# Optimization experiments

Hardware: AMD Instinct MI355X
Metric: run time of the kernel (lower is better)

## Reference

```python
import jax, jax.numpy as jnp
import numpy as np

DIM = 192
HEADS = 6
HIDDEN = 384  # int(DIM * 2.0)


def _ln(x, w, b):
    # WithBias LayerNorm over channel dim (torch normalizes last dim of b,(hw),c)
    mu = jnp.mean(x, axis=1, keepdims=True)
    var = jnp.var(x, axis=1, keepdims=True)
    return (x - mu) / jnp.sqrt(var + 1e-5) * w[None, :, None, None] + b[None, :, None, None]


def _conv1x1(x, w):  # w: [O, I, 1, 1]
    return jnp.einsum('bihw,oi->bohw', x, w[:, :, 0, 0])


def _dwconv3(x, w):  # depthwise 3x3, w: [C, 1, 3, 3]
    return jax.lax.conv_general_dilated(
        x, w, window_strides=(1, 1), padding=((1, 1), (1, 1)),
        feature_group_count=x.shape[1],
        dimension_numbers=('NCHW', 'OIHW', 'NCHW'))


def _l2norm(x):  # F.normalize along last axis
    n = jnp.sqrt(jnp.sum(x * x, axis=-1, keepdims=True))
    return x / jnp.maximum(n, 1e-12)


def setup_inputs() -> dict:
    key = jax.random.key(0)
    ks = jax.random.split(key, 16)
    s = 0.02
    d = {}
    d['x'] = jax.random.normal(ks[0], (2, DIM, 128, 128), dtype=jnp.float32)
    d['k_v'] = jax.random.normal(ks[1], (2, 256), dtype=jnp.float32)
    d['ln1_w'] = jnp.ones((DIM,), jnp.float32)
    d['ln1_b'] = jnp.zeros((DIM,), jnp.float32)
    d['temp'] = jnp.ones((HEADS, 1, 1), jnp.float32)
    d['w_kR'] = jax.random.normal(ks[2], (DIM * 3 // 4, 192), jnp.float32) * s
    d['w_kI'] = jax.random.normal(ks[3], (DIM // 4, 64), jnp.float32) * s
    d['w_qR'] = jax.random.normal(ks[4], (DIM, DIM * 3 // 4, 1, 1), jnp.float32) * s
    d['w_qdw'] = jax.random.normal(ks[5], (DIM, 1, 3, 3), jnp.float32) * s
    d['w_kvI'] = jax.random.normal(ks[6], (DIM * 2, DIM // 4, 1, 1), jnp.float32) * s
    d['w_kvdw'] = jax.random.normal(ks[7], (DIM * 2, 1, 3, 3), jnp.float32) * s
    d['w_po'] = jax.random.normal(ks[8], (DIM, DIM, 1, 1), jnp.float32) * s
    d['ln2_w'] = jnp.ones((DIM,), jnp.float32)
    d['ln2_b'] = jnp.zeros((DIM,), jnp.float32)
    d['w_ffk'] = jax.random.normal(ks[9], (DIM, 256), jnp.float32) * s
    d['w_pin'] = jax.random.normal(ks[10], (HIDDEN * 2, DIM, 1, 1), jnp.float32) * s
    d['w_dw'] = jax.random.normal(ks[11], (HIDDEN * 2, 1, 3, 3), jnp.float32) * s
    d['w_pout'] = jax.random.normal(ks[12], (DIM, HIDDEN, 1, 1), jnp.float32) * s
    return d


def reference(x, k_v, ln1_w, ln1_b, temp, w_kR, w_kI, w_qR, w_qdw, w_kvI, w_kvdw,
              w_po, ln2_w, ln2_b, w_ffk, w_pin, w_dw, w_pout):
    b, c, h, w = x.shape
    c3 = c * 3 // 4
    # ---- Rttention on norm1(x) ----
    xn = _ln(x, ln1_w, ln1_b)
    kvr = (k_v[:, :192] @ w_kR.T)[:, :, None, None]   # [b, 3c/4, 1, 1]
    kvi = (k_v[:, 192:] @ w_kI.T)[:, :, None, None]   # [b, c/4, 1, 1]
    x_r = xn[:, :c3] * kvr + xn[:, :c3]
    x_i = xn[:, c3:] * kvi + xn[:, c3:]
    q = _dwconv3(_conv1x1(x_r, w_qR), w_qdw)          # [b, c, h, w]
    kv = _dwconv3(_conv1x1(x_i, w_kvI), w_kvdw)       # [b, 2c, h, w]
    k, v = jnp.split(kv, 2, axis=1)
    rh = lambda t: t.reshape(b, HEADS, c // HEADS, h * w)
    q = _l2norm(rh(q))
    k = _l2norm(rh(k))
    v = rh(v)
    # channel-wise attention: [b, head, c_h, c_h]
    attn = jax.nn.softmax(jnp.einsum('bhcd,bhed->bhce', q, k) * temp[None], axis=-1)
    out = jnp.einsum('bhce,bhed->bhcd', attn, v).reshape(b, c, h, w)
    x = x + _conv1x1(out, w_po)
    # ---- GDFN FeedForward on norm2(x) ----
    xn2 = _ln(x, ln2_w, ln2_b)
    kvf = (k_v @ w_ffk.T)[:, :, None, None]           # [b, c, 1, 1]
    y = xn2 * kvf + xn2
    y = _dwconv3(_conv1x1(y, w_pin), w_dw)            # [b, 2*hidden, h, w]
    y1, y2 = jnp.split(y, 2, axis=1)
    y = jax.nn.gelu(y1, approximate=False) * y2
    x = x + _conv1x1(y, w_pout)
    return (x, k_v)
```

## Files before the change

kernel.cpp:

```cpp
#include <hip/hip_runtime.h>
#include <math.h>

#define HW 16384
#define CDIM 192
#define C3 144
#define C4 48
#define NB 2
#define NPX 32768
#define HEADS 6

typedef unsigned short u16;
typedef unsigned int u32;
typedef __attribute__((ext_vector_type(8))) short bf16x8;
typedef __attribute__((ext_vector_type(4))) float f32x4;

__device__ __forceinline__ float bf2f(u16 u) {
    return __uint_as_float(((unsigned int)u) << 16);
}
__device__ __forceinline__ u16 f2bf(float f) {
    unsigned int x = __float_as_uint(f);
    unsigned int r = x + 0x7fffu + ((x >> 16) & 1u);
    return (u16)(r >> 16);
}

static inline float* wsf(void* ws, size_t off) { return (float*)((char*)ws + off); }
static inline u16* wsh(void* ws, size_t off) { return (u16*)((char*)ws + off); }

__global__ void k_setup(const float* __restrict__ kvv, const float* __restrict__ wkR,
                        const float* __restrict__ wkI, const float* __restrict__ wffk,
                        const float* __restrict__ wqR, const float* __restrict__ wkvI,
                        const float* __restrict__ wpo, const float* __restrict__ wpin,
                        const float* __restrict__ wpout,
                        const float* __restrict__ ln2w, const float* __restrict__ ln2b,
                        u16* __restrict__ wb, float* __restrict__ sm,
                        float* __restrict__ A2, float* __restrict__ B2,
                        float* __restrict__ tail) {
    int t = blockIdx.x * 256 + threadIdx.x;
    if (t < 313344) {
        float v;
        if (t < 30720) {
            int o = t / 160, i = t % 160;
            v = (i < 144) ? wqR[o * 144 + i] : 0.f;
        } else if (t < 55296) {
            int r = t - 30720; int o = r / 64, i = r % 64;
            v = (i < 48) ? wkvI[o * 48 + i] : 0.f;
        } else if (t < 92160) {
            v = wpo[t - 55296];
        } else if (t < 239616) {
            v = wpin[t - 92160];
        } else {
            v = wpout[t - 239616];
        }
        wb[t] = f2bf(v);
    } else if (t < 314112) {
        int r = t - 313344;
        if (r < 288) {
            int b = r / 144, o = r % 144;
            const float* v = kvv + b * 256;
            const float* w = wkR + o * 192;
            float s = 0.f;
            for (int j = 0; j < 192; j++) s += v[j] * w[j];
            sm[r] = s + 1.0f;
        } else if (r < 384) {
            int r2 = r - 288;
            int b = r2 / 48, o = r2 % 48;
            const float* v = kvv + b * 256 + 192;
            const float* w = wkI + o * 64;
            float s = 0.f;
            for (int j = 0; j < 64; j++) s += v[j] * w[j];
            sm[288 + r2] = s + 1.0f;
        } else {
            int r2 = r - 384;
            int b = r2 / 192, o = r2 % 192;
            const float* v = kvv + b * 256;
            const float* w = wffk + o * 256;
            float s = 0.f;
            for (int j = 0; j < 256; j++) s += v[j] * w[j];
            float sc = s + 1.0f;
            sm[384 + r2] = sc;
            A2[r2] = ln2w[o] * sc;
            B2[r2] = ln2b[o] * sc;
        }
    } else if (t < 314624) {
        int r = t - 314112;
        tail[r] = kvv[r];
    }
}

__global__ __launch_bounds__(256) void k_ln1(
    const float* __restrict__ xin,
    const float* __restrict__ lnw, const float* __restrict__ lnb,
    const float* __restrict__ sca, const float* __restrict__ scb,
    u16* __restrict__ outA, u16* __restrict__ outB) {
    __shared__ float red[2][16][16][4];
    __shared__ float mu_s[16][4], rstd_s[16][4];
    int t = threadIdx.x;
    int px4 = t & 15, cg = t >> 4;
    int base = blockIdx.x * 64;
    int b = base >> 14;
    int p = (base & 16383) + px4 * 4;
    float vals[12][4];
    float s[4] = {0.f, 0.f, 0.f, 0.f}, s2[4] = {0.f, 0.f, 0.f, 0.f};
#pragma unroll
    for (int j = 0; j < 12; j++) {
        int c = cg * 12 + j;
        size_t off = ((size_t)(b * CDIM + c)) * HW + p;
        float4 f = *(const float4*)(xin + off);
        float v[4] = {f.x, f.y, f.z, f.w};
#pragma unroll
        for (int q = 0; q < 4; q++) {
            vals[j][q] = v[q]; s[q] += v[q]; s2[q] += v[q] * v[q];
        }
    }
#pragma unroll
    for (int q = 0; q < 4; q++) { red[0][cg][px4][q] = s[q]; red[1][cg][px4][q] = s2[q]; }
    __syncthreads();
    if (t < 16) {
        float S[4] = {0.f, 0.f, 0.f, 0.f}, S2[4] = {0.f, 0.f, 0.f, 0.f};
        for (int g2 = 0; g2 < 16; g2++)
#pragma unroll
            for (int q = 0; q < 4; q++) { S[q] += red[0][g2][t][q]; S2[q] += red[1][g2][t][q]; }
#pragma unroll
        for (int q = 0; q < 4; q++) {
            float mu = S[q] * (1.0f / CDIM);
            float var = S2[q] * (1.0f / CDIM) - mu * mu;
            mu_s[t][q] = mu;
            rstd_s[t][q] = rsqrtf(var + 1e-5f);
        }
    }
    __syncthreads();
    float mu[4], rs[4];
#pragma unroll
    for (int q = 0; q < 4; q++) { mu[q] = mu_s[px4][q]; rs[q] = rstd_s[px4][q]; }
    float Ac[12], Bc[12];
#pragma unroll
    for (int j = 0; j < 12; j++) {
        int c = cg * 12 + j;
        float sc = (c < C3) ? sca[b * C3 + c] : scb[b * C4 + (c - C3)];
        Ac[j] = lnw[c] * sc;
        Bc[j] = lnb[c] * sc;
    }
    int isR = (cg < 12);
    size_t row0 = (size_t)b * HW + p;
    u16* basep = isR ? (outA + row0 * 160 + cg * 12)
                     : (outB + row0 * 64 + (cg * 12 - 144));
    int rowlen = isR ? 160 : 64;
#pragma unroll
    for (int q = 0; q < 4; q++) {
        u16 tmp[12];
#pragma unroll
        for (int j = 0; j < 12; j++)
            tmp[j] = f2bf((vals[j][q] - mu[q]) * rs[q] * Ac[j] + Bc[j]);
        u16* op = basep + q * rowlen;
        ushort4 o0 = {tmp[0], tmp[1], tmp[2], tmp[3]};
        ushort4 o1 = {tmp[4], tmp[5], tmp[6], tmp[7]};
        ushort4 o2 = {tmp[8], tmp[9], tmp[10], tmp[11]};
        *(ushort4*)(op) = o0;
        *(ushort4*)(op + 4) = o1;
        *(ushort4*)(op + 8) = o2;
    }
    if (cg == 0) {
        int4 z = {0, 0, 0, 0};
#pragma unroll
        for (int q = 0; q < 4; q++) {
            u16* pr = outA + (row0 + q) * 160 + 144;
            *(int4*)(pr) = z; *(int4*)(pr + 8) = z;
            u16* pi = outB + (row0 + q) * 64 + 48;
            *(int4*)(pi) = z; *(int4*)(pi + 8) = z;
        }
    }
}

template <int NCH, int MODE>
__global__ __launch_bounds__(256) void k_gemm_t(
    const u16* __restrict__ X, const u16* __restrict__ Wb,
    const void* __restrict__ resid, void* __restrict__ outp, int CO) {
    constexpr int CIP = NCH * 32;
    const int tid = threadIdx.x;
    const int n0 = blockIdx.x * 128;
    const int m0 = blockIdx.y * 64;
    const int b = blockIdx.z;
    const int wave = tid >> 6, lane = tid & 63;
    const int quad = lane >> 4, l16 = lane & 15;
    const u16* arow = Wb + (size_t)(m0 + l16) * CIP + quad * 8;
    const u16* brow = X + ((size_t)b * HW + n0 + wave * 32 + l16) * CIP + quad * 8;
    f32x4 acc[4][2] = {};
#pragma unroll
    for (int ch = 0; ch < NCH; ch++) {
        const int k0 = ch * 32;
        bf16x8 bf0 = *(const bf16x8*)(brow + k0);
        bf16x8 bf1 = *(const bf16x8*)(brow + 16 * CIP + k0);
        bf16x8 af[4];
#pragma unroll
        for (int mi = 0; mi < 4; mi++)
            af[mi] = *(const bf16x8*)(arow + mi * 16 * CIP + k0);
#pragma unroll
        for (int mi = 0; mi < 4; mi++) {
            acc[mi][0] = __builtin_amdgcn_mfma_f32_16x16x32_bf16(af[mi], bf0, acc[mi][0], 0, 0, 0);
            acc[mi][1] = __builtin_amdgcn_mfma_f32_16x16x32_bf16(af[mi], bf1, acc[mi][1], 0, 0, 0);
        }
    }
#pragma unroll
    for (int mi = 0; mi < 4; mi++) {
#pragma unroll
        for (int ni = 0; ni < 2; ni++) {
            int c0 = m0 + mi * 16 + quad * 4;
            int px = n0 + wave * 32 + ni * 16 + l16;
            if (MODE == 0) {
                u16* ob = (u16*)outp + ((size_t)b * CO + c0) * HW + px;
#pragma unroll
                for (int r = 0; r < 4; r++) ob[(size_t)r * HW] = f2bf(acc[mi][ni][r]);
            } else {
                const float* rp = (const float*)resid + ((size_t)b * 192 + c0) * HW + px;
                ushort4 o;
                o.x = f2bf(acc[mi][ni][0] + rp[0]);
                o.y = f2bf(acc[mi][ni][1] + rp[(size_t)HW]);
                o.z = f2bf(acc[mi][ni][2] + rp[(size_t)2 * HW]);
                o.w = f2bf(acc[mi][ni][3] + rp[(size_t)3 * HW]);
                *(ushort4*)((u16*)outp + ((size_t)b * HW + px) * 192 + c0) = o;
            }
        }
    }
}

__global__ __launch_bounds__(256) void k_gemm_s(
    const u16* __restrict__ X, const u16* __restrict__ Wb,
    const u16* __restrict__ residT, float* __restrict__ outp) {
    constexpr int NCH = 12;
    constexpr int CIP = NCH * 32;
    __shared__ __align__(16) u16 Ws[64 * 32];
    __shared__ __align__(16) u16 Xs[32 * 130];
    const int tid = threadIdx.x;
    const int n0 = blockIdx.x * 128;
    const int m0 = blockIdx.y * 64;
    const int b = blockIdx.z;
    const u16* Xb = X + (size_t)b * 384 * HW + n0;
    const int wave = tid >> 6, lane = tid & 63;
    const int quad = lane >> 4, l16 = lane & 15;
    const int smr = tid >> 2, sk4 = tid & 3;
    const int skr = tid >> 3, sc0 = (tid & 7) * 16;
    f32x4 acc[4][2] = {};
    for (int ch = 0; ch < NCH; ch++) {
        const int k0 = ch * 32;
        if (ch) __syncthreads();
        {
            const int4 wv = *(const int4*)(Wb + (size_t)(m0 + smr) * CIP + k0 + sk4 * 8);
            *(int4*)&Ws[(smr << 5) + (((sk4 ^ (smr & 3)) & 3) << 3)] = wv;
        }
        {
            const u16* xc = Xb + (size_t)(k0 + skr) * HW + sc0;
            int4 r0 = *(const int4*)xc;
            int4 r1 = *(const int4*)(xc + 8);
            u32* dst = (u32*)&Xs[skr * 130 + sc0];
#pragma unroll
            for (int i = 0; i < 4; i++) dst[i] = ((const u32*)&r0)[i];
#pragma unroll
            for (int i = 0; i < 4; i++) dst[4 + i] = ((const u32*)&r1)[i];
        }
        __syncthreads();
        bf16x8 af[4];
#pragma unroll
        for (int mi = 0; mi < 4; mi++) {
            int row = mi * 16 + l16;
            af[mi] = *(const bf16x8*)&Ws[(row << 5) + ((quad ^ (row & 3)) << 3)];
        }
#pragma unroll
        for (int ni = 0; ni < 2; ni++) {
            int n = wave * 32 + ni * 16 + l16;
            bf16x8 bfr;
#pragma unroll
            for (int j = 0; j < 8; j++) bfr[j] = (short)Xs[(quad * 8 + j) * 130 + n];
#pragma unroll
            for (int mi = 0; mi < 4; mi++)
                acc[mi][ni] = __builtin_amdgcn_mfma_f32_16x16x32_bf16(af[mi], bfr, acc[mi][ni], 0, 0, 0);
        }
    }
#pragma unroll
    for (int mi = 0; mi < 4; mi++) {
#pragma unroll
        for (int ni = 0; ni < 2; ni++) {
            int c0 = m0 + mi * 16 + quad * 4;
            int px = n0 + wave * 32 + ni * 16 + l16;
            ushort4 rv = *(const ushort4*)(residT + ((size_t)b * HW + px) * 192 + c0);
            float* ob = outp + ((size_t)b * 192 + c0) * HW + px;
            ob[0] = acc[mi][ni][0] + bf2f(rv.x);
            ob[(size_t)HW] = acc[mi][ni][1] + bf2f(rv.y);
            ob[(size_t)2 * HW] = acc[mi][ni][2] + bf2f(rv.z);
            ob[(size_t)3 * HW] = acc[mi][ni][3] + bf2f(rv.w);
        }
    }
}

__global__ __launch_bounds__(256) void k_dw2(const u16* __restrict__ X,
                                             const float* __restrict__ Wd,
                                             u16* __restrict__ out, int C, int sqCh,
                                             float* __restrict__ sqp) {
    __shared__ float In[34 * 132];
    __shared__ float red[4];
    int bc = blockIdx.x >> 2, rt = blockIdx.x & 3;
    int b = bc / C, ch = bc % C;
    const u16* xb = X + (size_t)bc * HW;
    int t = threadIdx.x;
    int c0 = (t & 7) * 16;
    for (int r = t >> 3; r < 34; r += 32) {
        int y = rt * 32 - 1 + r;
        float* dst = &In[r * 132 + 1 + c0];
        if ((unsigned)y < 128u) {
            const u16* src = xb + y * 128 + c0;
            int4 r0 = *(const int4*)src;
            int4 r1 = *(const int4*)(src + 8);
            const u16* p0 = (const u16*)&r0;
            const u16* p1 = (const u16*)&r1;
#pragma unroll
            for (int i = 0; i < 8; i++) dst[i] = bf2f(p0[i]);
#pragma unroll
            for (int i = 0; i < 8; i++) dst[8 + i] = bf2f(p1[i]);
        } else {
#pragma unroll
            for (int i = 0; i < 16; i++) dst[i] = 0.f;
        }
    }
    if (t < 34) { In[t * 132] = 0.f; In[t * 132 + 129] = 0.f; }
    __syncthreads();
    const float* w = Wd + ch * 9;
    float w00 = w[0], w01 = w[1], w02 = w[2], w10 = w[3], w11 = w[4],
          w12 = w[5], w20 = w[6], w21 = w[7], w22 = w[8];
    int x = t & 127, rg = t >> 7;
    int base = rg * 16;
    float A2 = 0.f, A1 = 0.f, B1 = 0.f, ssq = 0.f;
    u16* ob = out + (size_t)bc * HW + (rt * 32 + base) * 128 + x;
#pragma unroll
    for (int r = 0; r < 18; r++) {
        const float* row = &In[(base + r) * 132 + x];
        float v0 = row[0], v1 = row[1], v2 = row[2];
        float h0 = w00 * v0 + w01 * v1 + w02 * v2;
        float h1 = w10 * v0 + w11 * v1 + w12 * v2;
        float h2 = w20 * v0 + w21 * v1 + w22 * v2;
        if (r >= 2) {
            float val = A2 + B1 + h2;
            ob[(size_t)(r - 2) * 128] = f2bf(val);
            ssq += val * val;
        }
        A2 = A1; A1 = h0; B1 = h1;
    }
    if (ch < sqCh) {
        for (int o = 32; o > 0; o >>= 1) ssq += __shfl_down(ssq, o, 64);
        int wid = t >> 6, lane = t & 63;
        if (lane == 0) red[wid] = ssq;
        __syncthreads();
        if (t == 0) sqp[((b * 192 + ch) << 2) | rt] = red[0] + red[1] + red[2] + red[3];
    }
}

__global__ __launch_bounds__(256) void k_dw_gelu2(const u16* __restrict__ G0,
                                                  const float* __restrict__ Wd,
                                                  u16* __restrict__ out) {
    __shared__ float In[2 * 34 * 132];
    int bc = blockIdx.x >> 2, rt = blockIdx.x & 3;
    int b = bc / 384, j = bc % 384;
    int t = threadIdx.x;
    int c0 = (t & 7) * 16;
    for (int pl = 0; pl < 2; pl++) {
        const u16* xb = G0 + ((size_t)b * 768 + pl * 384 + j) * HW;
        float* pla = &In[pl * 34 * 132];
        for (int r = t >> 3; r < 34; r += 32) {
            int y = rt * 32 - 1 + r;
            float* dst = &pla[r * 132 + 1 + c0];
            if ((unsigned)y < 128u) {
                const u16* src = xb + y * 128 + c0;
                int4 r0 = *(const int4*)src;
                int4 r1 = *(const int4*)(src + 8);
                const u16* p0 = (const u16*)&r0;
                const u16* p1 = (const u16*)&r1;
#pragma unroll
                for (int i = 0; i < 8; i++) dst[i] = bf2f(p0[i]);
#pragma unroll
                for (int i = 0; i < 8; i++) dst[8 + i] = bf2f(p1[i]);
            } else {
#pragma unroll
                for (int i = 0; i < 16; i++) dst[i] = 0.f;
            }
        }
        if (t < 34) { pla[t * 132] = 0.f; pla[t * 132 + 129] = 0.f; }
    }
    __syncthreads();
    const float* w1 = Wd + j * 9;
    const float* w2 = Wd + (384 + j) * 9;
    float a00 = w1[0], a01 = w1[1], a02 = w1[2], a10 = w1[3], a11 = w1[4],
          a12 = w1[5], a20 = w1[6], a21 = w1[7], a22 = w1[8];
    float b00 = w2[0], b01 = w2[1], b02 = w2[2], b10 = w2[3], b11 = w2[4],
          b12 = w2[5], b20 = w2[6], b21 = w2[7], b22 = w2[8];
    int x = t & 127, rg = t >> 7;
    int base = rg * 16;
    float A2a = 0.f, A1a = 0.f, B1a = 0.f;
    float A2b = 0.f, A1b = 0.f, B1b = 0.f;
    u16* ob = out + ((size_t)b * 384 + j) * HW + (rt * 32 + base) * 128 + x;
#pragma unroll
    for (int r = 0; r < 18; r++) {
        const float* r1p = &In[(base + r) * 132 + x];
        const float* r2p = r1p + 34 * 132;
        float u0 = r1p[0], u1 = r1p[1], u2 = r1p[2];
        float v0 = r2p[0], v1 = r2p[1], v2 = r2p[2];
        float h0a = a00 * u0 + a01 * u1 + a02 * u2;
        float h1a = a10 * u0 + a11 * u1 + a12 * u2;
        float h2a = a20 * u0 + a21 * u1 + a22 * u2;
        float h0b = b00 * v0 + b01 * v1 + b02 * v2;
        float h1b = b10 * v0 + b11 * v1 + b12 * v2;
        float h2b = b20 * v0 + b21 * v1 + b22 * v2;
        if (r >= 2) {
            float s1 = A2a + B1a + h2a;
            float s2 = A2b + B1b + h2b;
            float g = 0.5f * s1 * (1.0f + erff(s1 * 0.70710678118654752f));
            ob[(size_t)(r - 2) * 128] = f2bf(g * s2);
        }
        A2a = A1a; A1a = h0a; B1a = h1a;
        A2b = A1b; A1b = h0b; B1b = h1b;
    }
}

__global__ __launch_bounds__(256) void k_qk(const u16* __restrict__ qb_,
                                            const u16* __restrict__ kb_,
                                            float* __restrict__ Spart) {
    int bh = blockIdx.x >> 5, ds = blockIdx.x & 31;
    int b = bh / HEADS, h = bh % HEADS;
    int tid = threadIdx.x;
    int wave = tid >> 6, lane = tid & 63;
    int quad = lane >> 4, l16 = lane & 15;
    int tm = wave >> 1, tn = wave & 1;
    const u16* qrow = qb_ + ((size_t)(b * 192 + h * 32 + tm * 16 + l16)) * HW + ds * 512 + quad * 8;
    const u16* krow = kb_ + ((size_t)(b * 384 + h * 32 + tn * 16 + l16)) * HW + ds * 512 + quad * 8;
    f32x4 acc = {};
#pragma unroll
    for (int ch = 0; ch < 16; ch++) {
        bf16x8 a = *(const bf16x8*)(qrow + ch * 32);
        bf16x8 k8 = *(const bf16x8*)(krow + ch * 32);
        acc = __builtin_amdgcn_mfma_f32_16x16x32_bf16(a, k8, acc, 0, 0, 0);
    }
    float* Sb = Spart + ((size_t)ds * 12 + bh) * 1024;
#pragma unroll
    for (int r = 0; r < 4; r++)
        Sb[(tm * 16 + quad * 4 + r) * 32 + tn * 16 + l16] = acc[r];
}

__global__ void k_softmax(const float* __restrict__ Spart, const float* __restrict__ sqqp,
                          const float* __restrict__ sqkp, const float* __restrict__ temp,
                          u16* __restrict__ attnb) {
    int row = blockIdx.x;
    int bh = row >> 5, c2 = row & 31;
    int b = bh / HEADS, h = bh % HEADS;
    int e = threadIdx.x;
    float l = -1e30f;
    if (e < 32) {
        float s = 0.f;
        for (int d = 0; d < 32; d++) s += Spart[((size_t)d * 12 + bh) * 1024 + c2 * 32 + e];
        const float* qp = sqqp + (b * 192 + h * 32 + c2) * 4;
        const float* kp = sqkp + (b * 192 + h * 32 + e) * 4;
        float nq = qp[0] + qp[1] + qp[2] + qp[3];
        float nk = kp[0] + kp[1] + kp[2] + kp[3];
        float invq = 1.0f / fmaxf(sqrtf(nq), 1e-12f);
        float invk = 1.0f / fmaxf(sqrtf(nk), 1e-12f);
        l = s * invq * invk * temp[h];
    }
    float m = l;
    for (int o = 32; o > 0; o >>= 1) m = fmaxf(m, __shfl_xor(m, o, 64));
    float ev = (e < 32) ? expf(l - m) : 0.f;
    float ssum = ev;
    for (int o = 32; o > 0; o >>= 1) ssum += __shfl_xor(ssum, o, 64);
    if (e < 32) attnb[bh * 1024 + c2 * 32 + e] = f2bf(ev / ssum);
}

__global__ __launch_bounds__(256) void k_av(const u16* __restrict__ attnb,
                                            const u16* __restrict__ kvb,
                                            u16* __restrict__ out) {
    __shared__ __align__(16) u16 Vs[32 * 130];
    int bh = blockIdx.x >> 7;
    int pt = blockIdx.x & 127;
    int b = bh / HEADS, h = bh % HEADS;
    int p0 = pt * 128;
    int t = threadIdx.x;
    {
        int e = t >> 3, c0 = (t & 7) * 16;
        const u16* src = kvb + ((size_t)(b * 384 + 192 + h * 32 + e)) * HW + p0 + c0;
        int4 r0 = *(const int4*)src;
        int4 r1 = *(const int4*)(src + 8);
        u32* dst = (u32*)&Vs[e * 130 + c0];
#pragma unroll
        for (int i = 0; i < 4; i++) dst[i] = ((const u32*)&r0)[i];
#pragma unroll
        for (int i = 0; i < 4; i++) dst[4 + i] = ((const u32*)&r1)[i];
    }
    __syncthreads();
    int wave = t >> 6, lane = t & 63;
    int quad = lane >> 4, l16 = lane & 15;
    f32x4 acc[2][2] = {};
    bf16x8 af[2];
#pragma unroll
    for (int tm = 0; tm < 2; tm++)
        af[tm] = *(const bf16x8*)(attnb + bh * 1024 + (tm * 16 + l16) * 32 + quad * 8);
#pragma unroll
    for (int nt = 0; nt < 2; nt++) {
        int n = wave * 32 + nt * 16 + l16;
        bf16x8 bfr;
#pragma unroll
        for (int j = 0; j < 8; j++) bfr[j] = (short)Vs[(quad * 8 + j) * 130 + n];
#pragma unroll
        for (int tm = 0; tm < 2; tm++)
            acc[tm][nt] = __builtin_amdgcn_mfma_f32_16x16x32_bf16(af[tm], bfr, acc[tm][nt], 0, 0, 0);
    }
#pragma unroll
    for (int tm = 0; tm < 2; tm++)
#pragma unroll
        for (int nt = 0; nt < 2; nt++) {
            int c0 = h * 32 + tm * 16 + quad * 4;
            int px = p0 + wave * 32 + nt * 16 + l16;
            ushort4 o;
            o.x = f2bf(acc[tm][nt][0]);
            o.y = f2bf(acc[tm][nt][1]);
            o.z = f2bf(acc[tm][nt][2]);
            o.w = f2bf(acc[tm][nt][3]);
            *(ushort4*)(out + ((size_t)b * HW + px) * 192 + c0) = o;
        }
}

__global__ __launch_bounds__(256) void k_ln2t(
    const u16* __restrict__ xin, const float* __restrict__ A2,
    const float* __restrict__ B2, u16* __restrict__ outp) {
    int t = threadIdx.x;
    int pxg = blockIdx.x * 64 + (t >> 2);
    int l2 = t & 3;
    int b = pxg >> 14;
    const u16* src = xin + (size_t)pxg * 192 + l2 * 48;
    float v[48];
    float s = 0.f, s2 = 0.f;
#pragma unroll
    for (int i = 0; i < 6; i++) {
        int4 r0 = *(const int4*)(src + i * 8);
        const u16* pp = (const u16*)&r0;
#pragma unroll
        for (int k = 0; k < 8; k++) {
            float f = bf2f(pp[k]);
            v[i * 8 + k] = f; s += f; s2 += f * f;
        }
    }
    s += __shfl_xor(s, 1, 64);  s += __shfl_xor(s, 2, 64);
    s2 += __shfl_xor(s2, 1, 64); s2 += __shfl_xor(s2, 2, 64);
    float mu = s * (1.0f / CDIM);
    float rstd = rsqrtf(s2 * (1.0f / CDIM) - mu * mu + 1e-5f);
    const float* Ap = A2 + b * 192 + l2 * 48;
    const float* Bp = B2 + b * 192 + l2 * 48;
    u16* dst = outp + (size_t)pxg * 192 + l2 * 48;
#pragma unroll
    for (int i = 0; i < 12; i++) {
        float4 a = *(const float4*)(Ap + i * 4);
        float4 bb = *(const float4*)(Bp + i * 4);
        ushort4 o;
        o.x = f2bf((v[i * 4 + 0] - mu) * rstd * a.x + bb.x);
        o.y = f2bf((v[i * 4 + 1] - mu) * rstd * a.y + bb.y);
        o.z = f2bf((v[i * 4 + 2] - mu) * rstd * a.z + bb.z);
        o.w = f2bf((v[i * 4 + 3] - mu) * rstd * a.w + bb.w);
        *(ushort4*)(dst + i * 4) = o;
    }
}

extern "C" void kernel_launch(void* const* d_in, const int* in_sizes, int n_in,
                              void* d_out, int out_size, void* d_ws, size_t ws_size,
                              hipStream_t stream) {
    const float* x     = (const float*)d_in[0];
    const float* k_v   = (const float*)d_in[1];
    const float* ln1w  = (const float*)d_in[2];
    const float* ln1b  = (const float*)d_in[3];
    const float* temp  = (const float*)d_in[4];
    const float* w_kR  = (const float*)d_in[5];
    const float* w_kI  = (const float*)d_in[6];
    const float* w_qR  = (const float*)d_in[7];
    const float* w_qdw = (const float*)d_in[8];
    const float* w_kvI = (const float*)d_in[9];
    const float* w_kvdw= (const float*)d_in[10];
    const float* w_po  = (const float*)d_in[11];
    const float* ln2w  = (const float*)d_in[12];
    const float* ln2b  = (const float*)d_in[13];
    const float* w_ffk = (const float*)d_in[14];
    const float* w_pin = (const float*)d_in[15];
    const float* w_dw  = (const float*)d_in[16];
    const float* w_pout= (const float*)d_in[17];
    float* out = (float*)d_out;

    const size_t MiB = 1048576ULL;
    u16*   q0b     = wsh(d_ws, 0);
    u16*   attnoutb= wsh(d_ws, 0);
    u16*   y0b     = wsh(d_ws, 0);
    u16*   kv0b    = wsh(d_ws, 12 * MiB);
    u16*   ybufb   = wsh(d_ws, 12 * MiB);
    u16*   x1b     = wsh(d_ws, 36 * MiB);
    u16*   qbuf_b  = wsh(d_ws, 48 * MiB);
    u16*   kvbuf_b = wsh(d_ws, 60 * MiB);
    u16*   xrb     = wsh(d_ws, 84 * MiB);
    u16*   xib     = wsh(d_ws, 94 * MiB);
    u16*   g0b     = wsh(d_ws, 98 * MiB);
    u16*   wb      = wsh(d_ws, 146 * MiB);
    float* sm      = wsf(d_ws, 147 * MiB);
    float* Spart   = wsf(d_ws, 148 * MiB);
    u16* wq   = wb;
    u16* wkv  = wb + 30720;
    u16* wpo  = wb + 55296;
    u16* wpin = wb + 92160;
    u16* wpout= wb + 239616;
    float* kvr  = sm;
    float* kvi  = sm + 288;
    float* sqqp = sm + 768;
    float* sqkp = sm + 2304;
    u16*   attnb= (u16*)(sm + 3840);
    float* A2c  = sm + 10240;
    float* B2c  = sm + 10624;

    k_setup<<<1229, 256, 0, stream>>>(k_v, w_kR, w_kI, w_ffk, w_qR, w_kvI, w_po,
                                      w_pin, w_pout, ln2w, ln2b, wb, sm, A2c, B2c,
                                      out + (size_t)NB * CDIM * HW);
    k_ln1<<<NPX / 64, 256, 0, stream>>>(x, ln1w, ln1b, kvr, kvi, xrb, xib);
    k_gemm_t<5, 0><<<dim3(128, 3, 2), 256, 0, stream>>>(xrb, wq, nullptr, q0b, 192);
    k_gemm_t<2, 0><<<dim3(128, 6, 2), 256, 0, stream>>>(xib, wkv, nullptr, kv0b, 384);
    k_dw2<<<NB * 192 * 4, 256, 0, stream>>>(q0b, w_qdw, qbuf_b, 192, 192, sqqp);
    k_dw2<<<NB * 384 * 4, 256, 0, stream>>>(kv0b, w_kvdw, kvbuf_b, 384, 192, sqkp);
    k_qk<<<12 * 32, 256, 0, stream>>>(qbuf_b, kvbuf_b, Spart);
    k_softmax<<<384, 64, 0, stream>>>(Spart, sqqp, sqkp, temp, attnb);
    k_av<<<12 * 128, 256, 0, stream>>>(attnb, kvbuf_b, attnoutb);
    k_gemm_t<6, 1><<<dim3(128, 3, 2), 256, 0, stream>>>(attnoutb, wpo, x, x1b, 192);
    k_ln2t<<<NPX / 64, 256, 0, stream>>>(x1b, A2c, B2c, y0b);
    k_gemm_t<6, 0><<<dim3(128, 12, 2), 256, 0, stream>>>(y0b, wpin, nullptr, g0b, 768);
    k_dw_gelu2<<<NB * 384 * 4, 256, 0, stream>>>(g0b, w_dw, ybufb);
    k_gemm_s<<<dim3(128, 3, 2), 256, 0, stream>>>(ybufb, wpout, x1b, out);
}
```

Measured before the change: 306.7 us.

## Software-pipeline GEMM and QK loads, double QK split-K parallelism

The tiled GEMM kernel now keeps a three-slot register ring and issues global loads two K-chunks ahead of the MFMA work. It also gains a min-blocks-per-SM launch bound to improve latency hiding. The QK kernel splits the pixel dimension into 64 chunks instead of 32, giving twice as many blocks with a similar prefetch ring, and softmax reduces over 64 partials. Spart moves into the start of the workspace, which is assumed free at that point. Costs are higher register pressure and more partial-sum traffic in softmax.

```diff
diff --git a/kernel.cpp b/kernel.cpp
--- a/kernel.cpp
+++ b/kernel.cpp
@@ -172,7 +172,7 @@
 }
 
 template <int NCH, int MODE>
-__global__ __launch_bounds__(256) void k_gemm_t(
+__global__ __launch_bounds__(256, 4) void k_gemm_t(
     const u16* __restrict__ X, const u16* __restrict__ Wb,
     const void* __restrict__ resid, void* __restrict__ outp, int CO) {
     constexpr int CIP = NCH * 32;
@@ -185,19 +185,26 @@
     const u16* arow = Wb + (size_t)(m0 + l16) * CIP + quad * 8;
     const u16* brow = X + ((size_t)b * HW + n0 + wave * 32 + l16) * CIP + quad * 8;
     f32x4 acc[4][2] = {};
+    bf16x8 A[3][4], B[3][2];
+    auto gload = [&](int slot, int cc) {
+        const int k0 = cc * 32;
+        B[slot][0] = *(const bf16x8*)(brow + k0);
+        B[slot][1] = *(const bf16x8*)(brow + 16 * CIP + k0);
+        A[slot][0] = *(const bf16x8*)(arow + k0);
+        A[slot][1] = *(const bf16x8*)(arow + 16 * CIP + k0);
+        A[slot][2] = *(const bf16x8*)(arow + 32 * CIP + k0);
+        A[slot][3] = *(const bf16x8*)(arow + 48 * CIP + k0);
+    };
+    gload(0, 0);
+    gload(1, 1);
 #pragma unroll
     for (int ch = 0; ch < NCH; ch++) {
-        const int k0 = ch * 32;
-        bf16x8 bf0 = *(const bf16x8*)(brow + k0);
-        bf16x8 bf1 = *(const bf16x8*)(brow + 16 * CIP + k0);
-        bf16x8 af[4];
-#pragma unroll
-        for (int mi = 0; mi < 4; mi++)
-            af[mi] = *(const bf16x8*)(arow + mi * 16 * CIP + k0);
+        if (ch + 2 < NCH) gload((ch + 2) % 3, ch + 2);
+        const int s = ch % 3;
 #pragma unroll
         for (int mi = 0; mi < 4; mi++) {
-            acc[mi][0] = __builtin_amdgcn_mfma_f32_16x16x32_bf16(af[mi], bf0, acc[mi][0], 0, 0, 0);
-            acc[mi][1] = __builtin_amdgcn_mfma_f32_16x16x32_bf16(af[mi], bf1, acc[mi][1], 0, 0, 0);
+            acc[mi][0] = __builtin_amdgcn_mfma_f32_16x16x32_bf16(A[s][mi], B[s][0], acc[mi][0], 0, 0, 0);
+            acc[mi][1] = __builtin_amdgcn_mfma_f32_16x16x32_bf16(A[s][mi], B[s][1], acc[mi][1], 0, 0, 0);
         }
     }
 #pragma unroll
@@ -421,20 +428,25 @@
 __global__ __launch_bounds__(256) void k_qk(const u16* __restrict__ qb_,
                                             const u16* __restrict__ kb_,
                                             float* __restrict__ Spart) {
-    int bh = blockIdx.x >> 5, ds = blockIdx.x & 31;
+    int bh = blockIdx.x >> 6, ds = blockIdx.x & 63;
     int b = bh / HEADS, h = bh % HEADS;
     int tid = threadIdx.x;
     int wave = tid >> 6, lane = tid & 63;
     int quad = lane >> 4, l16 = lane & 15;
     int tm = wave >> 1, tn = wave & 1;
-    const u16* qrow = qb_ + ((size_t)(b * 192 + h * 32 + tm * 16 + l16)) * HW + ds * 512 + quad * 8;
-    const u16* krow = kb_ + ((size_t)(b * 384 + h * 32 + tn * 16 + l16)) * HW + ds * 512 + quad * 8;
+    const u16* qrow = qb_ + ((size_t)(b * 192 + h * 32 + tm * 16 + l16)) * HW + ds * 256 + quad * 8;
+    const u16* krow = kb_ + ((size_t)(b * 384 + h * 32 + tn * 16 + l16)) * HW + ds * 256 + quad * 8;
     f32x4 acc = {};
-#pragma unroll
-    for (int ch = 0; ch < 16; ch++) {
-        bf16x8 a = *(const bf16x8*)(qrow + ch * 32);
-        bf16x8 k8 = *(const bf16x8*)(krow + ch * 32);
-        acc = __builtin_amdgcn_mfma_f32_16x16x32_bf16(a, k8, acc, 0, 0, 0);
+    bf16x8 qa[3], ka[3];
+    auto ld = [&](int s, int cc) {
+        qa[s] = *(const bf16x8*)(qrow + cc * 32);
+        ka[s] = *(const bf16x8*)(krow + cc * 32);
+    };
+    ld(0, 0); ld(1, 1);
+#pragma unroll
+    for (int ch = 0; ch < 8; ch++) {
+        if (ch + 2 < 8) ld((ch + 2) % 3, ch + 2);
+        acc = __builtin_amdgcn_mfma_f32_16x16x32_bf16(qa[ch % 3], ka[ch % 3], acc, 0, 0, 0);
     }
     float* Sb = Spart + ((size_t)ds * 12 + bh) * 1024;
 #pragma unroll
@@ -452,7 +464,7 @@
     float l = -1e30f;
     if (e < 32) {
         float s = 0.f;
-        for (int d = 0; d < 32; d++) s += Spart[((size_t)d * 12 + bh) * 1024 + c2 * 32 + e];
+        for (int d = 0; d < 64; d++) s += Spart[((size_t)d * 12 + bh) * 1024 + c2 * 32 + e];
         const float* qp = sqqp + (b * 192 + h * 32 + c2) * 4;
         const float* kp = sqkp + (b * 192 + h * 32 + e) * 4;
         float nq = qp[0] + qp[1] + qp[2] + qp[3];
@@ -599,7 +611,7 @@
     u16*   g0b     = wsh(d_ws, 98 * MiB);
     u16*   wb      = wsh(d_ws, 146 * MiB);
     float* sm      = wsf(d_ws, 147 * MiB);
-    float* Spart   = wsf(d_ws, 148 * MiB);
+    float* Spart   = wsf(d_ws, 0);
     u16* wq   = wb;
     u16* wkv  = wb + 30720;
     u16* wpo  = wb + 55296;
@@ -621,7 +633,7 @@
     k_gemm_t<2, 0><<<dim3(128, 6, 2), 256, 0, stream>>>(xib, wkv, nullptr, kv0b, 384);
     k_dw2<<<NB * 192 * 4, 256, 0, stream>>>(q0b, w_qdw, qbuf_b, 192, 192, sqqp);
     k_dw2<<<NB * 384 * 4, 256, 0, stream>>>(kv0b, w_kvdw, kvbuf_b, 384, 192, sqkp);
-    k_qk<<<12 * 32, 256, 0, stream>>>(qbuf_b, kvbuf_b, Spart);
+    k_qk<<<12 * 64, 256, 0, stream>>>(qbuf_b, kvbuf_b, Spart);
     k_softmax<<<384, 64, 0, stream>>>(Spart, sqqp, sqkp, temp, attnb);
     k_av<<<12 * 128, 256, 0, stream>>>(attnb, kvbuf_b, attnoutb);
     k_gemm_t<6, 1><<<dim3(128, 3, 2), 256, 0, stream>>>(attnoutb, wpo, x, x1b, 192);
```

After: 311.4 us. Within noise of the previous version (+1.5%).
